# Kernel tuning notes

Hardware: AMD Instinct MI355X
Metric: run time of the kernel (lower is better)

The kernel has to match this reference:

```python
import jax, jax.numpy as jnp
import numpy as np

B, H, W, C = 8, 32, 32, 512
NUM_HEADS = 8
NUM_GROUPS = 32
EPS = 1e-5
SKIP_SCALE = 1.0
HEAD_DIM = C // NUM_HEADS


def setup_inputs() -> dict:
    key = jax.random.key(0)
    ks = jax.random.split(key, 7)
    fan_in, fan_out = C, 3 * C
    lim_qkv = np.sqrt(6.0 / (fan_in + fan_out))
    lim_out = 1e-5 * np.sqrt(6.0 / (C + C))
    return {
        "x": jax.random.normal(ks[0], (B, H, W, C), jnp.float32),
        "norm_scale": jnp.ones((C,), jnp.float32),
        "norm_bias": jnp.zeros((C,), jnp.float32),
        "qkv_kernel": jax.random.uniform(ks[1], (C, NUM_HEADS, 3 * HEAD_DIM), jnp.float32, -lim_qkv, lim_qkv),
        "qkv_bias": jnp.zeros((NUM_HEADS, 3 * HEAD_DIM), jnp.float32),
        "out_kernel": jax.random.uniform(ks[2], (NUM_HEADS, HEAD_DIM, C), jnp.float32, -lim_out, lim_out),
        "out_bias": jnp.zeros((C,), jnp.float32),
    }


def group_norm(x, scale, bias):
    # x: (B, S, C); normalize per-group over (S, C//G), flax GroupNorm semantics
    b, s, c = x.shape
    g = NUM_GROUPS
    xg = x.reshape(b, s, g, c // g)
    mean = jnp.mean(xg, axis=(1, 3), keepdims=True)
    var = jnp.var(xg, axis=(1, 3), keepdims=True)
    xg = (xg - mean) * jax.lax.rsqrt(var + EPS)
    return xg.reshape(b, s, c) * scale + bias


def reference(x, norm_scale, norm_bias, qkv_kernel, qkv_bias, out_kernel, out_bias):
    batch_dims = x.shape[:-3]
    h, w, c = x.shape[-3:]
    xi = x.reshape(-1, h * w, c)  # (B, S, C)
    out = group_norm(xi, norm_scale, norm_bias)
    # QKV projection: (B,S,C) x (C, NH, 3*HD) -> (B,S,NH,3*HD)
    qkv = jnp.einsum('bsc,chd->bshd', out, qkv_kernel) + qkv_bias
    q, k, v = jnp.split(qkv, 3, axis=-1)  # each (B,S,NH,HD)
    scale = 1.0 / jnp.sqrt(jnp.sqrt(jnp.asarray(HEAD_DIM, jnp.float32)))
    q = q * scale
    k = k * scale
    attn = jnp.einsum('bqhd,bkhd->bhqk', q, k)
    attn = jax.nn.softmax(attn, axis=-1)
    o = jnp.einsum('bhqk,bkhd->bqhd', attn, v)
    o = jnp.einsum('bqhd,hdc->bqc', o, out_kernel) + out_bias
    o = (o + xi) * SKIP_SCALE
    return o.reshape((*batch_dims, h, w, c))
```

## Files before the change

### kernel.cpp

```cpp
#include <hip/hip_runtime.h>
#include <stdint.h>

typedef __attribute__((ext_vector_type(8))) short short8;
typedef __attribute__((ext_vector_type(4))) float f32x4;
typedef __attribute__((ext_vector_type(16))) float f32x16;
typedef __attribute__((ext_vector_type(4))) unsigned int u32x4;
typedef unsigned short u16;
typedef unsigned int u32;

#define NBATCH 8
#define SLEN 1024
#define CDIM 512
#define NHEADS 8
#define HDIM 64
#define MROWS (NBATCH*SLEN)
#define NQKV (NHEADS*3*HDIM)
#define QK_SCALE 0.35355339059327373f

__device__ inline u16 f2bf(float f){
  union{float f; uint32_t i;} v; v.f=f;
  uint32_t r = v.i + 0x7fffu + ((v.i>>16)&1u);
  return (u16)(r>>16);
}

__device__ inline u32 pk2(float a, float b){
  u32 r;
  asm("v_cvt_pk_bf16_f32 %0, %1, %2" : "=v"(r) : "v"(a), "v"(b));
  return r;
}

__device__ __forceinline__ void gld16(const u16* g, u16* l){
  __builtin_amdgcn_global_load_lds(
    (const __attribute__((address_space(1))) void*)g,
    (__attribute__((address_space(3))) void*)l, 16, 0, 0);
}

__device__ __forceinline__ void prep_body(const float* __restrict__ w, u16* __restrict__ wt,
                                          int N, int blk, int t){
  int tk = blk / (N/64), tn = blk % (N/64);
  int k0 = tk*64, n0 = tn*64;
  __shared__ u16 lt[64][72];
  int row = t >> 2, slot = t & 3;
  const float* src = w + (size_t)(k0+row)*N + n0 + slot*16;
  #pragma unroll
  for (int j=0;j<16;++j)
    lt[row][slot*16+j] = f2bf(src[j]);
  __syncthreads();
  u16 tmp[16];
  #pragma unroll
  for (int j=0;j<16;++j) tmp[j] = lt[slot*16+j][row];
  *(u32x4*)(wt + (size_t)(n0+row)*512 + k0 + slot*16)     = *(u32x4*)tmp;
  *(u32x4*)(wt + (size_t)(n0+row)*512 + k0 + slot*16 + 8) = *(u32x4*)(tmp+8);
}

__global__ __launch_bounds__(256) void prep_all(const float* __restrict__ wqkv, const float* __restrict__ wout,
                                                u16* __restrict__ wqkv_t, u16* __restrict__ wout_t){
  int blk = blockIdx.x, t = threadIdx.x;
  if (blk < 8*(NQKV/64)) prep_body(wqkv, wqkv_t, NQKV, blk, t);
  else                   prep_body(wout, wout_t, CDIM, blk - 8*(NQKV/64), t);
}

__global__ __launch_bounds__(256) void gn_fused(const float* __restrict__ x,
                        const float* __restrict__ scale, const float* __restrict__ bias,
                        u16* __restrict__ xn){
  int bid = blockIdx.x;
  int b = bid >> 5, g = bid & 31;
  int t = threadIdx.x;
  const float* base = x + (size_t)b*SLEN*CDIM + g*16;
  u16* obase = xn + (size_t)b*SLEN*CDIM + g*16;
  float s1=0.f, s2=0.f;
  for (int s = t; s < SLEN; s += 256){
    const float4* p = (const float4*)(base + (size_t)s*CDIM);
    #pragma unroll
    for (int j=0;j<4;++j){
      float4 v = p[j];
      s1 += v.x+v.y+v.z+v.w;
      s2 += v.x*v.x + v.y*v.y + v.z*v.z + v.w*v.w;
    }
  }
  #pragma unroll
  for (int m=1;m<64;m<<=1){ s1 += __shfl_xor(s1,m); s2 += __shfl_xor(s2,m); }
  __shared__ float red[8];
  __shared__ float mv[2];
  int wid = t>>6;
  if ((t&63)==0){ red[wid*2]=s1; red[wid*2+1]=s2; }
  __syncthreads();
  if (t==0){
    float a=0,c=0;
    #pragma unroll
    for (int w2=0;w2<4;++w2){ a+=red[w2*2]; c+=red[w2*2+1]; }
    float mean = a*(1.f/16384.f);
    float var  = c*(1.f/16384.f) - mean*mean;
    mv[0] = mean; mv[1] = rsqrtf(var + 1e-5f);
  }
  __syncthreads();
  float mean = mv[0], rstd = mv[1];
  float sc[16], bi[16];
  #pragma unroll
  for (int j=0;j<16;++j){ sc[j] = scale[g*16+j]*rstd; bi[j] = bias[g*16+j] - mean*scale[g*16+j]*rstd; }
  for (int s = t; s < SLEN; s += 256){
    const float* xp = base + (size_t)s*CDIM;
    short8 o0, o1;
    #pragma unroll
    for (int j=0;j<16;++j){
      float v = xp[j]*sc[j] + bi[j];
      if (j<8) o0[j] = (short)f2bf(v); else o1[j-8] = (short)f2bf(v);
    }
    short8* dst = (short8*)(obase + (size_t)s*CDIM);
    dst[0]=o0; dst[1]=o1;
  }
}

#define BM 128
#define BN 128
#define BK 64

template<int EPI, int NT>
__global__ __launch_bounds__(256, 3) void gemm_bf16(
    const u16* __restrict__ A, const u16* __restrict__ Bt,
    const float* __restrict__ bias, const float* __restrict__ resid,
    float* __restrict__ outF,
    u16* __restrict__ qb, u16* __restrict__ kb, u16* __restrict__ vtb)
{
  const int K = CDIM;
  int t = threadIdx.x;
  int l = t & 63, wid = t >> 6;
  int g = l >> 4, c = l & 15;
  int wr = wid >> 1, wc = wid & 1;
  int nwg = gridDim.x;
  int cpx = nwg >> 3;
  int orig = blockIdx.x;
  int swz = (orig & 7)*cpx + (orig >> 3);
  int m0 = (swz / NT) * BM, n0 = (swz % NT) * BN;

  __shared__ __attribute__((aligned(16))) u16 ls[16384];
  char* lsAc = (char*)ls; char* lsBc = (char*)(ls + 8192);

  f32x4 acc[4][4];
  #pragma unroll
  for (int i=0;i<4;++i)
    #pragma unroll
    for(int j=0;j<4;++j) acc[i][j] = (f32x4)0.f;

  int lrow = l >> 3, slot = l & 7;
  int scol = ((slot ^ lrow) << 3);
  const int KT = K / BK;
  for (int kt=0; kt<KT; ++kt){
    __syncthreads();
    int kbo = kt*BK;
    #pragma unroll
    for (int q2=0; q2<4; ++q2){
      int row = wid*32 + q2*8 + lrow;
      gld16(A  + (size_t)(m0+row)*K + kbo + scol, ls        + (wid*4+q2)*512);
      gld16(Bt + (size_t)(n0+row)*K + kbo + scol, ls + 8192 + (wid*4+q2)*512);
    }
    asm volatile("s_waitcnt vmcnt(0)" ::: "memory");
    __syncthreads();
    #pragma unroll
    for (int kk=0; kk<2; ++kk){
      short8 af[4], bfr[4];
      #pragma unroll
      for (int i=0;i<4;++i){
        int rowA = wr*64 + i*16 + c;
        af[i]  = *(const short8*)(lsAc + rowA*128 + ((kk*4+g) ^ (rowA&7))*16);
        int rowB = wc*64 + i*16 + c;
        bfr[i] = *(const short8*)(lsBc + rowB*128 + ((kk*4+g) ^ (rowB&7))*16);
      }
      #pragma unroll
      for (int i=0;i<4;++i)
        #pragma unroll
        for (int j=0;j<4;++j)
          acc[i][j] = __builtin_amdgcn_mfma_f32_16x16x32_bf16(af[i], bfr[j], acc[i][j], 0,0,0);
    }
  }

  if (EPI == 0){
    int b = m0 >> 10, s0 = m0 & (SLEN-1);
    __syncthreads();
    u16* lsC = ls;
    #pragma unroll
    for (int i=0;i<4;++i){
      int rl0 = wr*64 + i*16 + g*4;
      #pragma unroll
      for (int j=0;j<4;++j){
        int cl = wc*64 + j*16 + c;
        int gcol = n0 + cl;
        int jj = gcol % 192;
        float sc_ = (jj < 128) ? QK_SCALE : 1.0f;
        float bv = bias[gcol];
        #pragma unroll
        for (int r=0;r<4;++r)
          lsC[(rl0+r)*128 + cl] = f2bf((acc[i][j][r] + bv)*sc_);
      }
    }
    __syncthreads();
    #pragma unroll
    for (int cc=0; cc<8; ++cc){
      int ch = cc*256 + t;
      int rl = ch >> 4, slot2 = ch & 15;
      int cl = slot2*8;
      int gcol = n0 + cl;
      int h = gcol / 192, jj = gcol % 192;
      int s = s0 + rl;
      u32x4 vv = *(const u32x4*)(lsC + rl*128 + cl);
      size_t rowb = ((size_t)(b*NHEADS+h))*SLEN + s;
      if (jj < 64)       __builtin_nontemporal_store(vv, (u32x4*)(qb + rowb*HDIM + jj));
      else if (jj < 128) __builtin_nontemporal_store(vv, (u32x4*)(kb + rowb*HDIM + (jj-64)));
    }
    int blk3 = (n0 >> 7) % 3;
    if (blk3 != 0){
      __syncthreads();
      u16* lsV = ls;
      #pragma unroll
      for (int i=0;i<4;++i){
        int rl0 = wr*64 + i*16 + g*4;
        #pragma unroll
        for (int j=0;j<4;++j){
          int cl = wc*64 + j*16 + c;
          int jj = (n0 + cl) % 192;
          if (jj >= 128){
            #pragma unroll
            for (int r=0;r<4;++r)
              lsV[(jj-128)*136 + rl0 + r] = f2bf(acc[i][j][r] + bias[n0+cl]);
          }
        }
      }
      __syncthreads();
      int hv = (n0 + ((blk3==1)?0:64)) / 192;
      size_t vbase = ((size_t)(b*NHEADS+hv))*HDIM*SLEN;
      #pragma unroll
      for (int cc=0; cc<4; ++cc){
        int chunk = cc*256 + t;
        int d = chunk >> 4, so = (chunk & 15)*8;
        u32x4 vv = *(const u32x4*)(lsV + d*136 + so);
        __builtin_nontemporal_store(vv, (u32x4*)(vtb + vbase + (size_t)d*SLEN + s0 + so));
      }
    }
  } else {
    #pragma unroll
    for (int i=0;i<4;++i){
      int grow = m0 + wr*64 + i*16 + g*4;
      #pragma unroll
      for (int j=0;j<4;++j){
        int gcol = n0 + wc*64 + j*16 + c;
        float bv = bias[gcol];
        #pragma unroll
        for (int r=0;r<4;++r){
          size_t off = (size_t)(grow+r)*CDIM + gcol;
          float rv = __builtin_nontemporal_load(&resid[off]);
          __builtin_nontemporal_store(acc[i][j][r] + bv + rv, &outF[off]);
        }
      }
    }
  }
}

#define PV_KS(PT, QOFF, V0, V1, KS) { \
    u32 A0 = pk2(PT[QOFF+0], PT[QOFF+1]); \
    u32 A1 = pk2(PT[QOFF+2], PT[QOFF+3]); \
    u32 B0 = pk2(PT[QOFF+4], PT[QOFF+5]); \
    u32 B1 = pk2(PT[QOFF+6], PT[QOFF+7]); \
    auto r0_ = __builtin_amdgcn_permlane32_swap((int)A0, (int)B0, false, false); \
    auto r1_ = __builtin_amdgcn_permlane32_swap((int)A1, (int)B1, false, false); \
    uint4 w; \
    w.x = (u32)r0_[0]; w.y = (u32)r1_[0]; w.z = (u32)r0_[1]; w.w = (u32)r1_[1]; \
    short8 fP; __builtin_memcpy(&fP, &w, 16); \
    o0 = __builtin_amdgcn_mfma_f32_32x32x16_bf16(V0[KS], fP, o0, 0,0,0); \
    o1 = __builtin_amdgcn_mfma_f32_32x32x16_bf16(V1[KS], fP, o1, 0,0,0); }

__global__ __launch_bounds__(256, 2) void attn_fused(const u16* __restrict__ qg,
  const u16* __restrict__ kg, const u16* __restrict__ vtg, u16* __restrict__ og)
{
  int bid = blockIdx.x;
  int nid = (bid & 7)*64 + (bid >> 3);
  int bh = nid >> 3, qi = nid & 7;
  int t = threadIdx.x, l = t & 63, wid = t >> 6;
  int q = l & 31, hi = l >> 5;
  int q0 = qi*128 + wid*32;

  __shared__ __attribute__((aligned(16))) u16 kl[4][4096];
  __shared__ __attribute__((aligned(16))) u16 vl[4][4096];

  const u16* qrow = qg + ((size_t)bh*SLEN + q0 + q)*HDIM + hi*8;
  short8 fQ[4];
  #pragma unroll
  for (int ds=0; ds<4; ++ds) fQ[ds] = *(const short8*)(qrow + ds*16);

  f32x16 o0, o1;
  #pragma unroll
  for (int r=0;r<16;++r){ o0[r]=0.f; o1[r]=0.f; }
  float mr = -1e30f, lsum = 0.f;

  const u16* kt_base = kg  + (size_t)bh*SLEN*HDIM;
  const u16* vt_base = vtg + (size_t)bh*HDIM*SLEN;
  int srow = l >> 3, sslot = l & 7;
  int scol8 = ((sslot ^ srow) << 3);

#define STAGE(BUF, KV) { \
    _Pragma("unroll") \
    for (int j=0;j<2;++j){ \
      int row = wid*16 + j*8 + srow; \
      int chunk = wid*2 + j; \
      gld16(kt_base + (size_t)((KV)*64 + row)*HDIM + scol8, &kl[BUF][chunk*512]); \
      gld16(vt_base + (size_t)row*SLEN + (KV)*64 + scol8,   &vl[BUF][chunk*512]); \
    } }

  STAGE(0, 0)
  STAGE(1, 1)
  STAGE(2, 2)
  STAGE(3, 3)

  int sl_q = q & 7;
  for (int p=0; p<8; ++p){
    if (p < 7) asm volatile("s_waitcnt vmcnt(8)" ::: "memory");
    else       asm volatile("s_waitcnt vmcnt(0)" ::: "memory");
    __syncthreads();
    int tA = 2*p, tB = 2*p+1;
    const u16* kA = &kl[tA&3][0]; const u16* kB = &kl[tB&3][0];
    const u16* vA = &vl[tA&3][0]; const u16* vB = &vl[tB&3][0];
    short8 fKA0[4], fKA1[4], fKB0[4], fKB1[4];
    #pragma unroll
    for (int ds=0; ds<4; ++ds){
      int sl = ((ds*2+hi) ^ sl_q) << 3;
      fKA0[ds] = *(const short8*)(kA + q*64 + sl);
      fKA1[ds] = *(const short8*)(kA + (q+32)*64 + sl);
      fKB0[ds] = *(const short8*)(kB + q*64 + sl);
      fKB1[ds] = *(const short8*)(kB + (q+32)*64 + sl);
    }
    f32x16 pA0, pA1, pB0, pB1;
    #pragma unroll
    for (int r=0;r<16;++r){ pA0[r]=0.f; pA1[r]=0.f; pB0[r]=0.f; pB1[r]=0.f; }
    __builtin_amdgcn_s_setprio(1);
    #pragma unroll
    for (int ds=0; ds<4; ++ds){
      pA0 = __builtin_amdgcn_mfma_f32_32x32x16_bf16(fKA0[ds], fQ[ds], pA0, 0,0,0);
      pB0 = __builtin_amdgcn_mfma_f32_32x32x16_bf16(fKB0[ds], fQ[ds], pB0, 0,0,0);
      pA1 = __builtin_amdgcn_mfma_f32_32x32x16_bf16(fKA1[ds], fQ[ds], pA1, 0,0,0);
      pB1 = __builtin_amdgcn_mfma_f32_32x32x16_bf16(fKB1[ds], fQ[ds], pB1, 0,0,0);
    }
    __builtin_amdgcn_s_setprio(0);
    short8 fVA0[4], fVA1[4], fVB0[4], fVB1[4];
    #pragma unroll
    for (int ks=0; ks<4; ++ks){
      int sl = ((ks*2+hi) ^ sl_q) << 3;
      fVA0[ks] = *(const short8*)(vA + q*64 + sl);
      fVA1[ks] = *(const short8*)(vA + (q+32)*64 + sl);
      fVB0[ks] = *(const short8*)(vB + q*64 + sl);
      fVB1[ks] = *(const short8*)(vB + (q+32)*64 + sl);
    }
    float a8[8];
    #pragma unroll
    for (int r=0;r<8;++r){
      float ma = fmaxf(fmaxf(pA0[r],pA0[r+8]), fmaxf(pA1[r],pA1[r+8]));
      float mb = fmaxf(fmaxf(pB0[r],pB0[r+8]), fmaxf(pB1[r],pB1[r+8]));
      a8[r] = fmaxf(ma, mb);
    }
    #pragma unroll
    for (int s=4;s>0;s>>=1)
      #pragma unroll
      for (int r=0;r<4;++r) if (r<s) a8[r] = fmaxf(a8[r], a8[r+s]);
    auto rm_ = __builtin_amdgcn_permlane32_swap(
        __builtin_bit_cast(int, a8[0]), __builtin_bit_cast(int, a8[0]), false, false);
    float tmax = fmaxf(a8[0], fmaxf(__builtin_bit_cast(float, rm_[0]),
                                    __builtin_bit_cast(float, rm_[1])));
    if (!__all(tmax <= mr + 8.0f)){
      float mn = fmaxf(mr, tmax);
      float alpha = __expf(mr - mn);
      mr = mn;
      lsum *= alpha;
      #pragma unroll
      for (int r=0;r<16;++r){ o0[r]*=alpha; o1[r]*=alpha; }
    }
    #pragma unroll
    for (int r=0;r<16;++r){
      pA0[r] = __expf(pA0[r]-mr); pA1[r] = __expf(pA1[r]-mr);
      pB0[r] = __expf(pB0[r]-mr); pB1[r] = __expf(pB1[r]-mr);
    }
    float s8[8];
    #pragma unroll
    for (int r=0;r<8;++r)
      s8[r] = ((pA0[r]+pA0[r+8]) + (pA1[r]+pA1[r+8]))
            + ((pB0[r]+pB0[r+8]) + (pB1[r]+pB1[r+8]));
    #pragma unroll
    for (int s=4;s>0;s>>=1)
      #pragma unroll
      for (int r=0;r<4;++r) if (r<s) s8[r] += s8[r+s];
    auto rs_ = __builtin_amdgcn_permlane32_swap(
        __builtin_bit_cast(int, s8[0]), __builtin_bit_cast(int, s8[0]), false, false);
    lsum += __builtin_bit_cast(float, rs_[0]) + __builtin_bit_cast(float, rs_[1]);
    __builtin_amdgcn_s_setprio(1);
    PV_KS(pA0, 0, fVA0, fVA1, 0)
    PV_KS(pA0, 8, fVA0, fVA1, 1)
    PV_KS(pA1, 0, fVA0, fVA1, 2)
    PV_KS(pA1, 8, fVA0, fVA1, 3)
    PV_KS(pB0, 0, fVB0, fVB1, 0)
    PV_KS(pB0, 8, fVB0, fVB1, 1)
    PV_KS(pB1, 0, fVB0, fVB1, 2)
    PV_KS(pB1, 8, fVB0, fVB1, 3)
    __builtin_amdgcn_s_setprio(0);
    __syncthreads();
    if (p < 6){
      STAGE((2*p+4)&3, 2*p+4)
      STAGE((2*p+5)&3, 2*p+5)
    }
  }

  float inv = 1.f / lsum;
  int b = bh >> 3, h = bh & 7;
  u16* obase = og + ((size_t)b*SLEN + q0 + q)*CDIM + h*HDIM;
  #pragma unroll
  for (int pr=0; pr<8; ++pr){
    int d = ((2*pr)&3) + 8*(pr>>1) + 4*hi;
    *(u32*)(obase + d)      = pk2(o0[2*pr]*inv, o0[2*pr+1]*inv);
    *(u32*)(obase + 32 + d) = pk2(o1[2*pr]*inv, o1[2*pr+1]*inv);
  }
}

extern "C" void kernel_launch(void* const* d_in, const int* in_sizes, int n_in,
                              void* d_out, int out_size, void* d_ws, size_t ws_size,
                              hipStream_t stream){
  const float* x      = (const float*)d_in[0];
  const float* nscale = (const float*)d_in[1];
  const float* nbias  = (const float*)d_in[2];
  const float* wqkv   = (const float*)d_in[3];
  const float* bqkv   = (const float*)d_in[4];
  const float* wout   = (const float*)d_in[5];
  const float* bout   = (const float*)d_in[6];
  float* out = (float*)d_out;

  char* ws = (char*)d_ws;
  size_t off = 0;
  auto alloc = [&](size_t bytes){ void* p = ws + off; off += (bytes + 255) & ~255ull; return p; };
  u16* wqkv_t = (u16*)alloc((size_t)NQKV*CDIM*2);
  u16* wout_t = (u16*)alloc((size_t)CDIM*CDIM*2);
  u16* xn     = (u16*)alloc((size_t)MROWS*CDIM*2);
  u16* qb     = (u16*)alloc((size_t)MROWS*CDIM*2);
  u16* kb     = (u16*)alloc((size_t)MROWS*CDIM*2);
  u16* vtb    = (u16*)alloc((size_t)MROWS*CDIM*2);
  u16* ob     = (u16*)alloc((size_t)MROWS*CDIM*2);

  prep_all<<<dim3(8*(NQKV/64) + 8*(CDIM/64)), dim3(256), 0, stream>>>(wqkv, wout, wqkv_t, wout_t);
  gn_fused<<<dim3(256), dim3(256), 0, stream>>>(x, nscale, nbias, xn);
  gemm_bf16<0,12><<<dim3(768), dim3(256), 0, stream>>>(xn, wqkv_t, bqkv, nullptr, nullptr, qb, kb, vtb);
  attn_fused<<<dim3(512), dim3(256), 0, stream>>>(qb, kb, vtb, ob);
  gemm_bf16<1,4><<<dim3(256), dim3(256), 0, stream>>>(ob, wout_t, bout, x, out, nullptr, nullptr, nullptr);
}
```

Baseline: 95.26 us.

## Fold softmax scale and log2e into Q, use raw exp2, split PV accumulators

Moves the full 1/sqrt(d) scale plus log2(e) onto Q in the QKV epilogue so the attention kernel can call v_exp_f32 directly instead of __expf. The rescale-deferral threshold is converted to log2 units to keep the original bound. It also splits each PV output accumulator into two independent MFMA chains to shorten the dependency chain, at the cost of extra VGPRs. Separately, the group-norm kernel moves to 512-thread blocks for more memory parallelism.

```diff
diff --git a/kernel.cpp b/kernel.cpp
--- a/kernel.cpp
+++ b/kernel.cpp
@@ -16,6 +16,8 @@
 #define MROWS (NBATCH*SLEN)
 #define NQKV (NHEADS*3*HDIM)
 #define QK_SCALE 0.35355339059327373f
+#define Q_SCALE_L2E 0.18033688011111793f
+#define DEFER_THR 11.541560327111707f
 
 __device__ inline u16 f2bf(float f){
   union{float f; uint32_t i;} v; v.f=f;
@@ -26,6 +28,12 @@
 __device__ inline u32 pk2(float a, float b){
   u32 r;
   asm("v_cvt_pk_bf16_f32 %0, %1, %2" : "=v"(r) : "v"(a), "v"(b));
+  return r;
+}
+
+__device__ inline float exp2r(float x){
+  float r;
+  asm("v_exp_f32 %0, %1" : "=v"(r) : "v"(x));
   return r;
 }
 
@@ -60,7 +68,7 @@
   else                   prep_body(wout, wout_t, CDIM, blk - 8*(NQKV/64), t);
 }
 
-__global__ __launch_bounds__(256) void gn_fused(const float* __restrict__ x,
+__global__ __launch_bounds__(512, 2) void gn_fused(const float* __restrict__ x,
                         const float* __restrict__ scale, const float* __restrict__ bias,
                         u16* __restrict__ xn){
   int bid = blockIdx.x;
@@ -69,7 +77,7 @@
   const float* base = x + (size_t)b*SLEN*CDIM + g*16;
   u16* obase = xn + (size_t)b*SLEN*CDIM + g*16;
   float s1=0.f, s2=0.f;
-  for (int s = t; s < SLEN; s += 256){
+  for (int s = t; s < SLEN; s += 512){
     const float4* p = (const float4*)(base + (size_t)s*CDIM);
     #pragma unroll
     for (int j=0;j<4;++j){
@@ -80,7 +88,7 @@
   }
   #pragma unroll
   for (int m=1;m<64;m<<=1){ s1 += __shfl_xor(s1,m); s2 += __shfl_xor(s2,m); }
-  __shared__ float red[8];
+  __shared__ float red[16];
   __shared__ float mv[2];
   int wid = t>>6;
   if ((t&63)==0){ red[wid*2]=s1; red[wid*2+1]=s2; }
@@ -88,7 +96,7 @@
   if (t==0){
     float a=0,c=0;
     #pragma unroll
-    for (int w2=0;w2<4;++w2){ a+=red[w2*2]; c+=red[w2*2+1]; }
+    for (int w2=0;w2<8;++w2){ a+=red[w2*2]; c+=red[w2*2+1]; }
     float mean = a*(1.f/16384.f);
     float var  = c*(1.f/16384.f) - mean*mean;
     mv[0] = mean; mv[1] = rsqrtf(var + 1e-5f);
@@ -98,7 +106,7 @@
   float sc[16], bi[16];
   #pragma unroll
   for (int j=0;j<16;++j){ sc[j] = scale[g*16+j]*rstd; bi[j] = bias[g*16+j] - mean*scale[g*16+j]*rstd; }
-  for (int s = t; s < SLEN; s += 256){
+  for (int s = t; s < SLEN; s += 512){
     const float* xp = base + (size_t)s*CDIM;
     short8 o0, o1;
     #pragma unroll
@@ -186,7 +194,7 @@
         int cl = wc*64 + j*16 + c;
         int gcol = n0 + cl;
         int jj = gcol % 192;
-        float sc_ = (jj < 128) ? QK_SCALE : 1.0f;
+        float sc_ = (jj < 64) ? Q_SCALE_L2E : 1.0f;
         float bv = bias[gcol];
         #pragma unroll
         for (int r=0;r<4;++r)
@@ -255,7 +263,7 @@
   }
 }
 
-#define PV_KS(PT, QOFF, V0, V1, KS) { \
+#define PV_KS(PT, QOFF, V0, V1, KS, OA, OB) { \
     u32 A0 = pk2(PT[QOFF+0], PT[QOFF+1]); \
     u32 A1 = pk2(PT[QOFF+2], PT[QOFF+3]); \
     u32 B0 = pk2(PT[QOFF+4], PT[QOFF+5]); \
@@ -265,8 +273,8 @@
     uint4 w; \
     w.x = (u32)r0_[0]; w.y = (u32)r1_[0]; w.z = (u32)r0_[1]; w.w = (u32)r1_[1]; \
     short8 fP; __builtin_memcpy(&fP, &w, 16); \
-    o0 = __builtin_amdgcn_mfma_f32_32x32x16_bf16(V0[KS], fP, o0, 0,0,0); \
-    o1 = __builtin_amdgcn_mfma_f32_32x32x16_bf16(V1[KS], fP, o1, 0,0,0); }
+    OA = __builtin_amdgcn_mfma_f32_32x32x16_bf16(V0[KS], fP, OA, 0,0,0); \
+    OB = __builtin_amdgcn_mfma_f32_32x32x16_bf16(V1[KS], fP, OB, 0,0,0); }
 
 __global__ __launch_bounds__(256, 2) void attn_fused(const u16* __restrict__ qg,
   const u16* __restrict__ kg, const u16* __restrict__ vtg, u16* __restrict__ og)
@@ -286,9 +294,9 @@
   #pragma unroll
   for (int ds=0; ds<4; ++ds) fQ[ds] = *(const short8*)(qrow + ds*16);
 
-  f32x16 o0, o1;
-  #pragma unroll
-  for (int r=0;r<16;++r){ o0[r]=0.f; o1[r]=0.f; }
+  f32x16 o0a, o0b, o1a, o1b;
+  #pragma unroll
+  for (int r=0;r<16;++r){ o0a[r]=0.f; o0b[r]=0.f; o1a[r]=0.f; o1b[r]=0.f; }
   float mr = -1e30f, lsum = 0.f;
 
   const u16* kt_base = kg  + (size_t)bh*SLEN*HDIM;
@@ -363,18 +371,18 @@
         __builtin_bit_cast(int, a8[0]), __builtin_bit_cast(int, a8[0]), false, false);
     float tmax = fmaxf(a8[0], fmaxf(__builtin_bit_cast(float, rm_[0]),
                                     __builtin_bit_cast(float, rm_[1])));
-    if (!__all(tmax <= mr + 8.0f)){
+    if (!__all(tmax <= mr + DEFER_THR)){
       float mn = fmaxf(mr, tmax);
-      float alpha = __expf(mr - mn);
+      float alpha = exp2r(mr - mn);
       mr = mn;
       lsum *= alpha;
       #pragma unroll
-      for (int r=0;r<16;++r){ o0[r]*=alpha; o1[r]*=alpha; }
+      for (int r=0;r<16;++r){ o0a[r]*=alpha; o0b[r]*=alpha; o1a[r]*=alpha; o1b[r]*=alpha; }
     }
     #pragma unroll
     for (int r=0;r<16;++r){
-      pA0[r] = __expf(pA0[r]-mr); pA1[r] = __expf(pA1[r]-mr);
-      pB0[r] = __expf(pB0[r]-mr); pB1[r] = __expf(pB1[r]-mr);
+      pA0[r] = exp2r(pA0[r]-mr); pA1[r] = exp2r(pA1[r]-mr);
+      pB0[r] = exp2r(pB0[r]-mr); pB1[r] = exp2r(pB1[r]-mr);
     }
     float s8[8];
     #pragma unroll
@@ -389,14 +397,14 @@
         __builtin_bit_cast(int, s8[0]), __builtin_bit_cast(int, s8[0]), false, false);
     lsum += __builtin_bit_cast(float, rs_[0]) + __builtin_bit_cast(float, rs_[1]);
     __builtin_amdgcn_s_setprio(1);
-    PV_KS(pA0, 0, fVA0, fVA1, 0)
-    PV_KS(pA0, 8, fVA0, fVA1, 1)
-    PV_KS(pA1, 0, fVA0, fVA1, 2)
-    PV_KS(pA1, 8, fVA0, fVA1, 3)
-    PV_KS(pB0, 0, fVB0, fVB1, 0)
-    PV_KS(pB0, 8, fVB0, fVB1, 1)
-    PV_KS(pB1, 0, fVB0, fVB1, 2)
-    PV_KS(pB1, 8, fVB0, fVB1, 3)
+    PV_KS(pA0, 0, fVA0, fVA1, 0, o0a, o1a)
+    PV_KS(pA0, 8, fVA0, fVA1, 1, o0a, o1a)
+    PV_KS(pA1, 0, fVA0, fVA1, 2, o0b, o1b)
+    PV_KS(pA1, 8, fVA0, fVA1, 3, o0b, o1b)
+    PV_KS(pB0, 0, fVB0, fVB1, 0, o0a, o1a)
+    PV_KS(pB0, 8, fVB0, fVB1, 1, o0a, o1a)
+    PV_KS(pB1, 0, fVB0, fVB1, 2, o0b, o1b)
+    PV_KS(pB1, 8, fVB0, fVB1, 3, o0b, o1b)
     __builtin_amdgcn_s_setprio(0);
     __syncthreads();
     if (p < 6){
@@ -411,8 +419,8 @@
   #pragma unroll
   for (int pr=0; pr<8; ++pr){
     int d = ((2*pr)&3) + 8*(pr>>1) + 4*hi;
-    *(u32*)(obase + d)      = pk2(o0[2*pr]*inv, o0[2*pr+1]*inv);
-    *(u32*)(obase + 32 + d) = pk2(o1[2*pr]*inv, o1[2*pr+1]*inv);
+    *(u32*)(obase + d)      = pk2((o0a[2*pr]+o0b[2*pr])*inv, (o0a[2*pr+1]+o0b[2*pr+1])*inv);
+    *(u32*)(obase + 32 + d) = pk2((o1a[2*pr]+o1b[2*pr])*inv, (o1a[2*pr+1]+o1b[2*pr+1])*inv);
   }
 }
 
@@ -440,7 +448,7 @@
   u16* ob     = (u16*)alloc((size_t)MROWS*CDIM*2);
 
   prep_all<<<dim3(8*(NQKV/64) + 8*(CDIM/64)), dim3(256), 0, stream>>>(wqkv, wout, wqkv_t, wout_t);
-  gn_fused<<<dim3(256), dim3(256), 0, stream>>>(x, nscale, nbias, xn);
+  gn_fused<<<dim3(256), dim3(512), 0, stream>>>(x, nscale, nbias, xn);
   gemm_bf16<0,12><<<dim3(768), dim3(256), 0, stream>>>(xn, wqkv_t, bqkv, nullptr, nullptr, qb, kb, vtb);
   attn_fused<<<dim3(512), dim3(256), 0, stream>>>(qb, kb, vtb, ob);
   gemm_bf16<1,4><<<dim3(256), dim3(256), 0, stream>>>(ob, wout_t, bout, x, out, nullptr, nullptr, nullptr);
```

After: 91.94 us. 1.04x faster.
